# Performance work log

Hardware: AMD Instinct MI355X
Metric: run time of the kernel (lower is better)

## Reference

```python
import jax, jax.numpy as jnp
import numpy as np

NUM_CLASSES = 1000
Z_DIM = 256
BATCH = 16384


def setup_inputs() -> dict:
    key = jax.random.key(0)
    k1, k2, k3 = jax.random.split(key, 3)
    x = jax.random.normal(k1, (BATCH, Z_DIM), dtype=jnp.float32)
    centers = jax.random.normal(k2, (NUM_CLASSES, Z_DIM), dtype=jnp.float32)
    labels = jax.random.randint(k3, (BATCH,), 0, NUM_CLASSES, dtype=jnp.int64)
    return {"x": x, "centers": centers, "labels": labels}


def reference(x, centers, labels):
    B, C = x.shape[0], centers.shape[0]
    distmat = (
        jnp.sum(x * x, axis=1, keepdims=True)
        + jnp.sum(centers * centers, axis=1)[None, :]
        - 2.0 * jnp.einsum("bd,cd->bc", x, centers)
    )
    # original gathers distances to NON-matching classes (kk = 1 - mask),
    # exactly C-1 entries per row, then sqrt, clamp, and global mean.
    mask = labels[:, None] == jnp.arange(C, dtype=labels.dtype)[None, :]  # True where class == label
    d = jnp.clip(jnp.sqrt(distmat), 1e-8, 1e8)
    total = jnp.sum(jnp.where(mask, 0.0, d))
    loss = total / (B * (C - 1))
    return loss
```

## Files before the change

kernel.cpp:

```cpp
#include <hip/hip_runtime.h>

#define BATCH 16384
#define ZDIM  256
#define NCLS  1000
#define NPAD  1024

typedef float f32x4 __attribute__((ext_vector_type(4)));

#define WS_XQ   0
#define WS_CQ   4194304
#define WS_XSQ  4456448
#define WS_CSQ  4521984
#define WS_PART 4526080

#define GLOAD_LDS(gp, lp)                                                     \
    __builtin_amdgcn_global_load_lds(                                         \
        (__attribute__((address_space(1))) const void*)(gp),                  \
        (__attribute__((address_space(3))) void*)(lp), 16, 0, 0)

template <bool W>
__device__ __forceinline__ int pk2fp8(float a, float b, int old) {
    return __builtin_amdgcn_cvt_pk_fp8_f32(a, b, old, W);
}

__global__ void prep(const float* __restrict__ x,
                     const float* __restrict__ centers,
                     char* __restrict__ xq,
                     char* __restrict__ cq,
                     float* __restrict__ xsq,
                     float* __restrict__ csq) {
    const int wid  = threadIdx.x >> 6;
    const int lane = threadIdx.x & 63;
    const int lr   = lane & 15;
    const int quad = lane >> 4;

    if (blockIdx.x < 256) {
        const int mt = blockIdx.x * 4 + wid;
        const float* src = x + (size_t)(mt * 16 + lr) * ZDIM + quad * 8;
        float s = 0.0f;
        #pragma unroll
        for (int kt = 0; kt < 8; ++kt) {
            const float4 a = *(const float4*)(src + kt * 32);
            const float4 b = *(const float4*)(src + kt * 32 + 4);
            s += a.x*a.x + a.y*a.y + a.z*a.z + a.w*a.w
               + b.x*b.x + b.y*b.y + b.z*b.z + b.w*b.w;
            int lo = pk2fp8<false>(a.x, a.y, 0); lo = pk2fp8<true>(a.z, a.w, lo);
            int hi = pk2fp8<false>(b.x, b.y, 0); hi = pk2fp8<true>(b.z, b.w, hi);
            int2 v; v.x = lo; v.y = hi;
            *(int2*)(xq + ((size_t)(mt * 8 + kt) * 64 + lane) * 8) = v;
        }
        s += __shfl_xor(s, 16);
        s += __shfl_xor(s, 32);
        if (lane < 16) xsq[mt * 16 + lane] = s;
    } else {
        const int ct  = (blockIdx.x - 256) * 4 + wid;
        const int row = ct * 16 + lr;
        const bool ok = (row < NCLS);
        const float* src = centers + (size_t)row * ZDIM + quad * 8;
        float s = 0.0f;
        #pragma unroll
        for (int kt = 0; kt < 8; ++kt) {
            float4 a = {0,0,0,0}, b = {0,0,0,0};
            if (ok) {
                a = *(const float4*)(src + kt * 32);
                b = *(const float4*)(src + kt * 32 + 4);
            }
            s += a.x*a.x + a.y*a.y + a.z*a.z + a.w*a.w
               + b.x*b.x + b.y*b.y + b.z*b.z + b.w*b.w;
            int lo = pk2fp8<false>(a.x, a.y, 0); lo = pk2fp8<true>(a.z, a.w, lo);
            int hi = pk2fp8<false>(b.x, b.y, 0); hi = pk2fp8<true>(b.z, b.w, hi);
            int2 v; v.x = lo; v.y = hi;
            *(int2*)(cq + ((size_t)(ct * 8 + kt) * 64 + lane) * 8) = v;
        }
        s += __shfl_xor(s, 16);
        s += __shfl_xor(s, 32);
        if (lane < 16) csq[ct * 16 + lane] = s;
    }
}

__global__ __launch_bounds__(512, 2) void gemm_loss(
        const char* __restrict__ xq,
        const char* __restrict__ cq,
        const float* __restrict__ xsq,
        const float* __restrict__ csq,
        const int* __restrict__ labels,
        float* __restrict__ part) {
    __shared__ char smem[65536];

    const int tid  = threadIdx.x;
    const int lane = tid & 63;
    const int wid  = tid >> 6;
    const int bm   = blockIdx.x & 63;
    const int bn   = blockIdx.x >> 6;
    const int m0   = bm * 256;
    const int n0   = bn * 256;
    const int wr   = wid & 3;
    const int wc   = wid >> 2;

    f32x4 acc_r[4][8];
    #pragma unroll
    for (int i = 0; i < 4; ++i)
        #pragma unroll
        for (int j = 0; j < 8; ++j) {
            f32x4 z = {0.0f, 0.0f, 0.0f, 0.0f};
            acc_r[i][j] = z;
        }

    const long long* AL = (const long long*)smem;
    const long long* BL = (const long long*)(smem + 32768);

    #pragma unroll
    for (int h = 0; h < 2; ++h) {
        #pragma unroll
        for (int it = 0; it < 4; ++it) {
            const int c = it * 512 + tid;
            const int mtile = c >> 7, kt4 = (c >> 5) & 3, pair = c & 31;
            const char* g = xq + (size_t)((bm * 16 + mtile) * 8 + h * 4 + kt4) * 512
                               + pair * 16;
            GLOAD_LDS(g, smem + c * 16);
        }
        #pragma unroll
        for (int it = 0; it < 4; ++it) {
            const int c = it * 512 + tid;
            const int ctile = c >> 7, kt4 = (c >> 5) & 3, pair = c & 31;
            const char* g = cq + (size_t)((bn * 16 + ctile) * 8 + h * 4 + kt4) * 512
                               + pair * 16;
            GLOAD_LDS(g, smem + 32768 + c * 16);
        }
        __syncthreads();

        #pragma unroll
        for (int kt4 = 0; kt4 < 4; ++kt4) {
            long long af[4], bf[8];
            #pragma unroll
            for (int mi = 0; mi < 4; ++mi)
                af[mi] = AL[((wr * 4 + mi) * 4 + kt4) * 64 + lane];
            #pragma unroll
            for (int nj = 0; nj < 8; ++nj)
                bf[nj] = BL[((wc * 8 + nj) * 4 + kt4) * 64 + lane];
            #pragma unroll
            for (int mi = 0; mi < 4; ++mi)
                #pragma unroll
                for (int nj = 0; nj < 8; ++nj)
                    acc_r[mi][nj] = __builtin_amdgcn_mfma_f32_16x16x32_fp8_fp8(
                        af[mi], bf[nj], acc_r[mi][nj], 0, 0, 0);
        }
        __syncthreads();
    }

    float* xsq_s = (float*)smem;
    float* csq_s = (float*)(smem + 1024);
    int*   lab_s = (int*)(smem + 2048);
    float* wsum  = (float*)(smem + 3072);
    if (tid < 256) {
        xsq_s[tid] = xsq[m0 + tid];
        lab_s[tid] = labels[m0 + tid];
    } else {
        const int t = tid - 256;
        csq_s[t] = csq[n0 + t];
    }
    __syncthreads();

    const int quad = lane >> 4;
    const int lr   = lane & 15;
    float sum = 0.0f;
    #pragma unroll
    for (int nj = 0; nj < 8; ++nj) {
        const int col_l = wc * 128 + nj * 16 + lr;
        const int col_g = n0 + col_l;
        const float cs = csq_s[col_l];
        const bool colok = (col_g < NCLS);
        #pragma unroll
        for (int mi = 0; mi < 4; ++mi) {
            #pragma unroll
            for (int r = 0; r < 4; ++r) {
                const int row_l = wr * 64 + mi * 16 + quad * 4 + r;
                float dist = xsq_s[row_l] + cs - 2.0f * acc_r[mi][nj][r];
                float d = sqrtf(fmaxf(dist, 0.0f));
                d = fminf(fmaxf(d, 1e-8f), 1e8f);
                if (colok && (lab_s[row_l] != col_g)) sum += d;
            }
        }
    }

    #pragma unroll
    for (int off = 32; off; off >>= 1) sum += __shfl_down(sum, off);
    if (lane == 0) wsum[wid] = sum;
    __syncthreads();
    if (tid == 0) {
        float t = 0.0f;
        #pragma unroll
        for (int w = 0; w < 8; ++w) t += wsum[w];
        part[blockIdx.x] = t;
    }
}

__global__ void finalize(const float* __restrict__ part, float* __restrict__ out) {
    const int tid  = threadIdx.x;
    const int lane = tid & 63;
    const int wid  = tid >> 6;
    __shared__ float wsum[4];
    float s = part[tid];
    #pragma unroll
    for (int off = 32; off; off >>= 1) s += __shfl_down(s, off);
    if (lane == 0) wsum[wid] = s;
    __syncthreads();
    if (tid == 0)
        out[0] = (wsum[0] + wsum[1] + wsum[2] + wsum[3]) * (1.0f / (16384.0f * 999.0f));
}

extern "C" void kernel_launch(void* const* d_in, const int* in_sizes, int n_in,
                              void* d_out, int out_size, void* d_ws, size_t ws_size,
                              hipStream_t stream) {
    const float* x       = (const float*)d_in[0];
    const float* centers = (const float*)d_in[1];
    const int*   labels  = (const int*)d_in[2];
    float*       out     = (float*)d_out;

    char* ws = (char*)d_ws;
    char*  xq   = ws + WS_XQ;
    char*  cq   = ws + WS_CQ;
    float* xsq  = (float*)(ws + WS_XSQ);
    float* csq  = (float*)(ws + WS_CSQ);
    float* part = (float*)(ws + WS_PART);

    prep<<<272, 256, 0, stream>>>(x, centers, xq, cq, xsq, csq);
    gemm_loss<<<256, 512, 0, stream>>>(xq, cq, xsq, csq, labels, part);
    finalize<<<1, 256, 0, stream>>>(part, out);
}
```

Before: 94.57 us.

## Fuse prep and GEMM-loss kernels via cooperative launch with grid sync

Merges the FP8 quantization/norm prep kernel into the GEMM-loss kernel and uses a cooperative launch with a grid-wide barrier between the phases. Each block quantizes a slice of x (4 waves) and some blocks also quantize center tiles, then all blocks sync and run the GEMM. This removes one kernel launch and the gap between kernels. It relies on all 256 blocks being co-resident and adds the cost of a grid barrier.

```diff
diff --git a/kernel.cpp b/kernel.cpp
--- a/kernel.cpp
+++ b/kernel.cpp
@@ -1,4 +1,7 @@
 #include <hip/hip_runtime.h>
+#include <hip/hip_cooperative_groups.h>
+
+namespace cg = cooperative_groups;
 
 #define BATCH 16384
 #define ZDIM  256
@@ -23,52 +26,61 @@
     return __builtin_amdgcn_cvt_pk_fp8_f32(a, b, old, W);
 }
 
-__global__ void prep(const float* __restrict__ x,
-                     const float* __restrict__ centers,
-                     char* __restrict__ xq,
-                     char* __restrict__ cq,
-                     float* __restrict__ xsq,
-                     float* __restrict__ csq) {
-    const int wid  = threadIdx.x >> 6;
-    const int lane = threadIdx.x & 63;
+__global__ __launch_bounds__(512, 2) void fused(
+        const float* __restrict__ x,
+        const float* __restrict__ centers,
+        const int* __restrict__ labels,
+        char* __restrict__ xq,
+        char* __restrict__ cq,
+        float* __restrict__ xsq,
+        float* __restrict__ csq,
+        float* __restrict__ part) {
+    __shared__ char smem[65536];
+
+    const int tid  = threadIdx.x;
+    const int lane = tid & 63;
+    const int wid  = tid >> 6;
+    const int b    = blockIdx.x;
+    const int bm   = b & 63;
+    const int bn   = b >> 6;
     const int lr   = lane & 15;
     const int quad = lane >> 4;
 
-    if (blockIdx.x < 256) {
-        const int mt = blockIdx.x * 4 + wid;
+    if (wid < 4) {
+        const int mt = bm * 16 + bn * 4 + wid;
         const float* src = x + (size_t)(mt * 16 + lr) * ZDIM + quad * 8;
         float s = 0.0f;
         #pragma unroll
         for (int kt = 0; kt < 8; ++kt) {
             const float4 a = *(const float4*)(src + kt * 32);
-            const float4 b = *(const float4*)(src + kt * 32 + 4);
+            const float4 c = *(const float4*)(src + kt * 32 + 4);
             s += a.x*a.x + a.y*a.y + a.z*a.z + a.w*a.w
-               + b.x*b.x + b.y*b.y + b.z*b.z + b.w*b.w;
+               + c.x*c.x + c.y*c.y + c.z*c.z + c.w*c.w;
             int lo = pk2fp8<false>(a.x, a.y, 0); lo = pk2fp8<true>(a.z, a.w, lo);
-            int hi = pk2fp8<false>(b.x, b.y, 0); hi = pk2fp8<true>(b.z, b.w, hi);
+            int hi = pk2fp8<false>(c.x, c.y, 0); hi = pk2fp8<true>(c.z, c.w, hi);
             int2 v; v.x = lo; v.y = hi;
             *(int2*)(xq + ((size_t)(mt * 8 + kt) * 64 + lane) * 8) = v;
         }
         s += __shfl_xor(s, 16);
         s += __shfl_xor(s, 32);
         if (lane < 16) xsq[mt * 16 + lane] = s;
-    } else {
-        const int ct  = (blockIdx.x - 256) * 4 + wid;
+    } else if (wid == 4 && bn == 0) {
+        const int ct  = bm;
         const int row = ct * 16 + lr;
         const bool ok = (row < NCLS);
         const float* src = centers + (size_t)row * ZDIM + quad * 8;
         float s = 0.0f;
         #pragma unroll
         for (int kt = 0; kt < 8; ++kt) {
-            float4 a = {0,0,0,0}, b = {0,0,0,0};
+            float4 a = {0,0,0,0}, c = {0,0,0,0};
             if (ok) {
                 a = *(const float4*)(src + kt * 32);
-                b = *(const float4*)(src + kt * 32 + 4);
+                c = *(const float4*)(src + kt * 32 + 4);
             }
             s += a.x*a.x + a.y*a.y + a.z*a.z + a.w*a.w
-               + b.x*b.x + b.y*b.y + b.z*b.z + b.w*b.w;
+               + c.x*c.x + c.y*c.y + c.z*c.z + c.w*c.w;
             int lo = pk2fp8<false>(a.x, a.y, 0); lo = pk2fp8<true>(a.z, a.w, lo);
-            int hi = pk2fp8<false>(b.x, b.y, 0); hi = pk2fp8<true>(b.z, b.w, hi);
+            int hi = pk2fp8<false>(c.x, c.y, 0); hi = pk2fp8<true>(c.z, c.w, hi);
             int2 v; v.x = lo; v.y = hi;
             *(int2*)(cq + ((size_t)(ct * 8 + kt) * 64 + lane) * 8) = v;
         }
@@ -76,26 +88,13 @@
         s += __shfl_xor(s, 32);
         if (lane < 16) csq[ct * 16 + lane] = s;
     }
-}
-
-__global__ __launch_bounds__(512, 2) void gemm_loss(
-        const char* __restrict__ xq,
-        const char* __restrict__ cq,
-        const float* __restrict__ xsq,
-        const float* __restrict__ csq,
-        const int* __restrict__ labels,
-        float* __restrict__ part) {
-    __shared__ char smem[65536];
-
-    const int tid  = threadIdx.x;
-    const int lane = tid & 63;
-    const int wid  = tid >> 6;
-    const int bm   = blockIdx.x & 63;
-    const int bn   = blockIdx.x >> 6;
-    const int m0   = bm * 256;
-    const int n0   = bn * 256;
-    const int wr   = wid & 3;
-    const int wc   = wid >> 2;
+
+    cg::this_grid().sync();
+
+    const int m0 = bm * 256;
+    const int n0 = bn * 256;
+    const int wr = wid & 3;
+    const int wc = wid >> 2;
 
     f32x4 acc_r[4][8];
     #pragma unroll
@@ -161,8 +160,6 @@
     }
     __syncthreads();
 
-    const int quad = lane >> 4;
-    const int lr   = lane & 15;
     float sum = 0.0f;
     #pragma unroll
     for (int nj = 0; nj < 8; ++nj) {
@@ -224,7 +221,10 @@
     float* csq  = (float*)(ws + WS_CSQ);
     float* part = (float*)(ws + WS_PART);
 
-    prep<<<272, 256, 0, stream>>>(x, centers, xq, cq, xsq, csq);
-    gemm_loss<<<256, 512, 0, stream>>>(xq, cq, xsq, csq, labels, part);
+    void* args[] = {(void*)&x, (void*)&centers, (void*)&labels,
+                    (void*)&xq, (void*)&cq, (void*)&xsq, (void*)&csq,
+                    (void*)&part};
+    hipLaunchCooperativeKernel((const void*)fused, dim3(256), dim3(512),
+                               args, 0, stream);
     finalize<<<1, 256, 0, stream>>>(part, out);
 }
```

Measured after the change: 131.6 us. 1.39x slower.
